# Kernel tuning notes

Measured on AMD Instinct MI355X. Metric: run time of the kernel, lower is better.

The kernel has to match this reference:

```python
import jax, jax.numpy as jnp
import numpy as np

N_NODES = 10000
N_EDGES = 160000
IN_DIM = 512
HID = 128
HEADS = 8
EMB = 256
NEG_SLOPE = 0.2  # PyG GATConv default


def setup_inputs() -> dict:
    key = jax.random.key(0)
    ks = jax.random.split(key, 12)
    x = jax.random.normal(ks[0], (N_NODES, IN_DIM), dtype=jnp.float32)
    edge_index = jax.random.randint(ks[1], (2, N_EDGES), 0, N_NODES, dtype=jnp.int64)
    s1 = 1.0 / np.sqrt(IN_DIM)
    s2 = 1.0 / np.sqrt(HEADS * HID)
    W1 = jax.random.normal(ks[2], (IN_DIM, HEADS * HID), dtype=jnp.float32) * s1
    a_src1 = jax.random.normal(ks[3], (HEADS, HID), dtype=jnp.float32) * s2
    a_dst1 = jax.random.normal(ks[4], (HEADS, HID), dtype=jnp.float32) * s2
    b1 = jnp.zeros((HEADS * HID,), dtype=jnp.float32)
    W2 = jax.random.normal(ks[5], (HEADS * HID, EMB), dtype=jnp.float32) * s2
    a_src2 = jax.random.normal(ks[6], (1, EMB), dtype=jnp.float32) * (1.0 / np.sqrt(EMB))
    a_dst2 = jax.random.normal(ks[7], (1, EMB), dtype=jnp.float32) * (1.0 / np.sqrt(EMB))
    b2 = jnp.zeros((EMB,), dtype=jnp.float32)
    return {"x": x, "edge_index": edge_index, "W1": W1, "a_src1": a_src1,
            "a_dst1": a_dst1, "b1": b1, "W2": W2, "a_src2": a_src2,
            "a_dst2": a_dst2, "b2": b2}


def gat_layer(h_in, src, dst, W, a_src, a_dst, b, concat, num_nodes):
    """PyG-style GATConv (eval mode, self-loops already in src/dst)."""
    H, C = a_src.shape
    h = (h_in @ W).reshape(num_nodes, H, C)            # [N, H, C]
    alpha_src = jnp.einsum('nhc,hc->nh', h, a_src)      # [N, H]
    alpha_dst = jnp.einsum('nhc,hc->nh', h, a_dst)      # [N, H]
    e = jax.nn.leaky_relu(alpha_src[src] + alpha_dst[dst], NEG_SLOPE)  # [E, H]
    # segment softmax over incoming edges of each destination node
    m = jax.ops.segment_max(e, dst, num_segments=num_nodes)            # [N, H]
    ex = jnp.exp(e - m[dst])
    denom = jax.ops.segment_sum(ex, dst, num_segments=num_nodes)       # [N, H]
    alpha = ex / denom[dst]                                            # [E, H]
    out = jax.ops.segment_sum(h[src] * alpha[:, :, None], dst,
                              num_segments=num_nodes)                  # [N, H, C]
    out = out.reshape(num_nodes, H * C) if concat else out.mean(axis=1)
    return out + b


def reference(x, edge_index, W1, a_src1, a_dst1, b1, W2, a_src2, a_dst2, b2):
    N = x.shape[0]
    loops = jnp.arange(N, dtype=edge_index.dtype)
    src = jnp.concatenate([edge_index[0], loops])
    dst = jnp.concatenate([edge_index[1], loops])
    h = gat_layer(x, src, dst, W1, a_src1, a_dst1, b1, concat=True, num_nodes=N)
    h = jax.nn.elu(h)  # dropout inactive in eval mode
    out = gat_layer(h, src, dst, W2, a_src2, a_dst2, b2, concat=False, num_nodes=N)
    return out
```

## Files before the change

kernel.cpp:

```cpp
#include <hip/hip_runtime.h>
#include <hip/hip_bf16.h>

typedef __attribute__((ext_vector_type(8))) short short8;
typedef __attribute__((ext_vector_type(4))) float floatx4;
typedef __attribute__((ext_vector_type(4))) unsigned short ushort4v;
typedef __attribute__((ext_vector_type(8))) unsigned short ushort8v;
typedef __attribute__((ext_vector_type(2))) unsigned int uint2v;
typedef __attribute__((ext_vector_type(4))) unsigned int uint4v;

#define NN 10000
#define E0 160000
#define ETOT (E0 + NN)
#define IN_DIM 512
#define HID1 1024
#define EMB 256
#define MPAD 10112
#define NX (NN * IN_DIM)
#define NW1 (IN_DIM * HID1)
#define NW2 (HID1 * EMB)
#define DETB 625

__device__ __forceinline__ float bf2f(unsigned short u) {
    unsigned v = ((unsigned)u) << 16;
    float f;
    __builtin_memcpy(&f, &v, 4);
    return f;
}
__device__ __forceinline__ float bflo(unsigned v) {
    unsigned x = v << 16;
    float f; __builtin_memcpy(&f, &x, 4);
    return f;
}
__device__ __forceinline__ float bfhi(unsigned v) {
    unsigned x = v & 0xffff0000u;
    float f; __builtin_memcpy(&f, &x, 4);
    return f;
}
__device__ __forceinline__ unsigned short f2bf(float f) {
    unsigned u;
    __builtin_memcpy(&u, &f, 4);
    unsigned lsb = (u >> 16) & 1;
    u += 0x7fff + lsb;
    return (unsigned short)(u >> 16);
}
__device__ __forceinline__ unsigned packbf(float lo, float hi) {
    return (unsigned)f2bf(lo) | ((unsigned)f2bf(hi) << 16);
}
__device__ __forceinline__ float loadf(const void* p, size_t i, int isf32) {
    if (isf32) return ((const float*)p)[i];
    return bf2f(((const unsigned short*)p)[i]);
}
__device__ __forceinline__ float lrelu(float e) { return e > 0.f ? e : 0.2f * e; }

__global__ void zero_kernel(int* p, int n) {
    int i = blockIdx.x * 256 + threadIdx.x;
    if (i < n) p[i] = 0;
}

__global__ __launch_bounds__(256) void probe_kernel(const int* ei32, const unsigned* xw,
                                                    int* eflag, int* isf32) {
    int t = threadIdx.x;
    if (blockIdx.x < DETB) {
        int i = blockIdx.x * 256 + t;
        int v = 0;
        int idx = 2 * i + 1;
        if (idx < 2 * E0) v = ei32[idx];
        unsigned long long any = __ballot(v != 0);
        if (any && (t & 63) == 0) atomicOr(eflag, 1);
    } else {
        __shared__ int cnt[256];
        int c = 0;
        #pragma unroll
        for (int j = 0; j < 16; ++j) {
            unsigned w = xw[t * 16 + j];
            int ex = (w >> 7) & 0xFF;
            if (ex >= 110 && ex <= 135) c++;
        }
        cnt[t] = c;
        __syncthreads();
        for (int off = 128; off > 0; off >>= 1) {
            if (t < off) cnt[t] += cnt[t + off];
            __syncthreads();
        }
        if (t == 0) *isf32 = (cnt[0] < 2048) ? 1 : 0;
    }
}

__device__ __forceinline__ int load_edge(const void* ei, long long idx, int m32) {
    if (m32) return ((const int*)ei)[idx];
    return (int)(((const long long*)ei)[idx]);
}

__global__ void count_kernel(const void* ei, const int* flag, int* counts) {
    int e = blockIdx.x * 256 + threadIdx.x;
    if (e < E0) {
        int m32 = (*flag != 0);
        int d = load_edge(ei, (long long)E0 + e, m32);
        if (d >= 0 && d < NN) atomicAdd(&counts[d], 1);
    }
}

__global__ __launch_bounds__(1024) void scan_kernel(const int* counts, int* offsets, int* cursor) {
    __shared__ int wsum[16];
    int t = threadIdx.x;
    int lane = t & 63, wv = t >> 6;
    int base = t * 10;
    int local[10];
    int s = 0;
    #pragma unroll
    for (int j = 0; j < 10; ++j) {
        int idx = base + j;
        int v = (idx < NN) ? (counts[idx] + 1) : 0;
        local[j] = v; s += v;
    }
    int v = s;
    #pragma unroll
    for (int d = 1; d < 64; d <<= 1) {
        int o = __shfl_up(v, d, 64);
        if (lane >= d) v += o;
    }
    if (lane == 63) wsum[wv] = v;
    __syncthreads();
    if (t < 16) {
        int w = wsum[t];
        #pragma unroll
        for (int d = 1; d < 16; d <<= 1) {
            int o = __shfl_up(w, d, 16);
            if (t >= d) w += o;
        }
        wsum[t] = w;
    }
    __syncthreads();
    int woff = (wv == 0) ? 0 : wsum[wv - 1];
    int run = woff + v - s;
    #pragma unroll
    for (int j = 0; j < 10; ++j) {
        int idx = base + j;
        if (idx < NN) { offsets[idx] = run; cursor[idx] = run; run += local[j]; }
    }
    if (t == 1023) offsets[NN] = wsum[15];
}

__global__ void scatter_kernel(const void* ei, const int* flag, int* cursor, int* csr_src) {
    int e = blockIdx.x * 256 + threadIdx.x;
    if (e >= ETOT) return;
    int m32 = (*flag != 0);
    int s, d;
    if (e < E0) { s = load_edge(ei, e, m32); d = load_edge(ei, (long long)E0 + e, m32); }
    else { s = d = e - E0; }
    if (s < 0) s = 0; if (s >= NN) s = NN - 1;
    if (d < 0) d = 0; if (d >= NN) d = NN - 1;
    int pos = atomicAdd(&cursor[d], 1);
    if (pos >= 0 && pos < ETOT) csr_src[pos] = s;
}

__global__ void convall_kernel(const void* x, const void* W1, const void* W2,
                               unsigned short* xb, unsigned short* W1t, unsigned short* W2t,
                               const int* isf32)
{
    int i = blockIdx.x * 256 + threadIdx.x;
    int f = *isf32;
    if (i < NX) { xb[i] = f2bf(loadf(x, i, f)); return; }
    i -= NX;
    if (i < NW1) {
        int r = i / HID1, c = i % HID1;
        W1t[(size_t)c * IN_DIM + r] = f2bf(loadf(W1, i, f));
        return;
    }
    i -= NW1;
    if (i < NW2) {
        int r = i / EMB, c = i % EMB;
        W2t[(size_t)c * HID1 + r] = f2bf(loadf(W2, i, f));
    }
}

template<bool OUTBF16>
__global__ __launch_bounds__(256) void gemm_tile(
    const unsigned short* __restrict__ A,
    const unsigned short* __restrict__ Bt,
    void* __restrict__ Cv,
    int N, int K)
{
    __shared__ unsigned short As[128 * 32];
    __shared__ unsigned short Bs[128 * 32];
    int t = threadIdx.x;
    int wave = t >> 6;
    int lane = t & 63;
    int quad = lane >> 4;
    int l16  = lane & 15;
    int mq = wave & 1, nq = wave >> 1;
    size_t mblk = (size_t)blockIdx.x * 128;
    size_t nblk = (size_t)blockIdx.y * 128;

    floatx4 acc[4][4];
    #pragma unroll
    for (int i = 0; i < 4; ++i)
        #pragma unroll
        for (int j = 0; j < 4; ++j)
            acc[i][j] = (floatx4){0.f, 0.f, 0.f, 0.f};

    const unsigned short* Abase = A + mblk * K;
    const unsigned short* Bbase = Bt + nblk * K;

    for (int kk = 0; kk < K; kk += 32) {
        __syncthreads();
        #pragma unroll
        for (int j = 0; j < 2; ++j) {
            int chunk = (wave << 7) + (j << 6) + lane;
            int r  = chunk >> 2;
            int cs = (chunk & 3) ^ (r & 3);
            const unsigned short* ga = Abase + (size_t)r * K + kk + cs * 8;
            const unsigned short* gb = Bbase + (size_t)r * K + kk + cs * 8;
            __builtin_amdgcn_global_load_lds(
                (const __attribute__((address_space(1))) void*)ga,
                (__attribute__((address_space(3))) void*)(As + (size_t)((wave << 7) + (j << 6)) * 8),
                16, 0, 0);
            __builtin_amdgcn_global_load_lds(
                (const __attribute__((address_space(1))) void*)gb,
                (__attribute__((address_space(3))) void*)(Bs + (size_t)((wave << 7) + (j << 6)) * 8),
                16, 0, 0);
        }
        __syncthreads();

        short8 af[4], bf[4];
        #pragma unroll
        for (int i = 0; i < 4; ++i) {
            int ar = mq * 64 + i * 16 + l16;
            int br = nq * 64 + i * 16 + l16;
            af[i] = *(const short8*)(const void*)(As + ar * 32 + (quad ^ (ar & 3)) * 8);
            bf[i] = *(const short8*)(const void*)(Bs + br * 32 + (quad ^ (br & 3)) * 8);
        }
        #pragma unroll
        for (int i = 0; i < 4; ++i)
            #pragma unroll
            for (int j = 0; j < 4; ++j)
                acc[i][j] = __builtin_amdgcn_mfma_f32_16x16x32_bf16(af[i], bf[j], acc[i][j], 0, 0, 0);
    }

    size_t crow0 = mblk + mq * 64 + quad * 4;
    size_t ccol0 = nblk + nq * 64 + l16;
    #pragma unroll
    for (int i = 0; i < 4; ++i) {
        #pragma unroll
        for (int r = 0; r < 4; ++r) {
            size_t row = crow0 + i * 16 + r;
            size_t b = row * N + ccol0;
            #pragma unroll
            for (int j = 0; j < 4; ++j) {
                if (OUTBF16) ((unsigned short*)Cv)[b + j * 16] = f2bf(acc[i][j][r]);
                else         ((float*)Cv)[b + j * 16] = acc[i][j][r];
            }
        }
    }
}

__global__ __launch_bounds__(256) void alpha1_kernel(
    const unsigned short* __restrict__ h1,
    const void* __restrict__ a_src, const void* __restrict__ a_dst,
    const int* __restrict__ isf32,
    float* __restrict__ as1, float* __restrict__ ad1)
{
    int n = blockIdx.x, t = threadIdx.x;
    int f = *isf32;
    ushort4v hv = *(const ushort4v*)(const void*)(h1 + (size_t)n * HID1 + t * 4);
    float ps = 0.f, pd = 0.f;
    #pragma unroll
    for (int i = 0; i < 4; ++i) {
        float h = bf2f(hv[i]);
        ps += h * loadf(a_src, t * 4 + i, f);
        pd += h * loadf(a_dst, t * 4 + i, f);
    }
    #pragma unroll
    for (int off = 1; off < 32; off <<= 1) {
        ps += __shfl_xor(ps, off, 64);
        pd += __shfl_xor(pd, off, 64);
    }
    if ((t & 31) == 0) {
        int h = t >> 5;
        as1[n * 8 + h] = ps;
        ad1[n * 8 + h] = pd;
    }
}

__global__ __launch_bounds__(256) void agg1_kernel(
    const unsigned short* __restrict__ h1, const int* __restrict__ offsets,
    const int* __restrict__ csr_src, const float* __restrict__ as1,
    const float* __restrict__ ad1, const void* __restrict__ b1,
    const int* __restrict__ isf32,
    unsigned short* __restrict__ hmid)
{
    int n = blockIdx.x, t = threadIdx.x;
    int f = *isf32;
    int beg = offsets[n], end = offsets[n + 1];
    if (beg < 0) beg = 0; if (end > ETOT) end = ETOT;
    int g = t >> 6;
    int u = t & 63;
    int c0 = u * 16;
    int hc = u >> 3;
    float ad = ad1[n * 8 + hc];
    const unsigned* rb = (const unsigned*)h1 + u * 8;

    float den = 0.f;
    float acc[16];
    #pragma unroll
    for (int j = 0; j < 16; ++j) acc[j] = 0.f;

    int i = beg + g;
    for (; i + 12 < end; i += 16) {
        int s0 = csr_src[i];      s0 &= 0x7fffffff; if (s0 >= NN) s0 = 0;
        int s1 = csr_src[i + 4];  s1 &= 0x7fffffff; if (s1 >= NN) s1 = 0;
        int s2 = csr_src[i + 8];  s2 &= 0x7fffffff; if (s2 >= NN) s2 = 0;
        int s3 = csr_src[i + 12]; s3 &= 0x7fffffff; if (s3 >= NN) s3 = 0;
        uint4v a0 = *(const uint4v*)(const void*)(rb + (size_t)s0 * 512);
        uint4v b0 = *(const uint4v*)(const void*)(rb + (size_t)s0 * 512 + 4);
        uint4v a1 = *(const uint4v*)(const void*)(rb + (size_t)s1 * 512);
        uint4v b1v = *(const uint4v*)(const void*)(rb + (size_t)s1 * 512 + 4);
        uint4v a2 = *(const uint4v*)(const void*)(rb + (size_t)s2 * 512);
        uint4v b2v = *(const uint4v*)(const void*)(rb + (size_t)s2 * 512 + 4);
        uint4v a3 = *(const uint4v*)(const void*)(rb + (size_t)s3 * 512);
        uint4v b3v = *(const uint4v*)(const void*)(rb + (size_t)s3 * 512 + 4);
        float w0 = __expf(lrelu(as1[s0 * 8 + hc] + ad));
        float w1 = __expf(lrelu(as1[s1 * 8 + hc] + ad));
        float w2 = __expf(lrelu(as1[s2 * 8 + hc] + ad));
        float w3 = __expf(lrelu(as1[s3 * 8 + hc] + ad));
        den += (w0 + w1) + (w2 + w3);
        #pragma unroll
        for (int q = 0; q < 4; ++q) {
            acc[2 * q]      += (bflo(a0[q]) * w0 + bflo(a1[q]) * w1) + (bflo(a2[q]) * w2 + bflo(a3[q]) * w3);
            acc[2 * q + 1]  += (bfhi(a0[q]) * w0 + bfhi(a1[q]) * w1) + (bfhi(a2[q]) * w2 + bfhi(a3[q]) * w3);
            acc[8 + 2 * q]  += (bflo(b0[q]) * w0 + bflo(b1v[q]) * w1) + (bflo(b2v[q]) * w2 + bflo(b3v[q]) * w3);
            acc[9 + 2 * q]  += (bfhi(b0[q]) * w0 + bfhi(b1v[q]) * w1) + (bfhi(b2v[q]) * w2 + bfhi(b3v[q]) * w3);
        }
    }
    for (; i + 4 < end; i += 8) {
        int s0 = csr_src[i];     s0 &= 0x7fffffff; if (s0 >= NN) s0 = 0;
        int s1 = csr_src[i + 4]; s1 &= 0x7fffffff; if (s1 >= NN) s1 = 0;
        uint4v a0 = *(const uint4v*)(const void*)(rb + (size_t)s0 * 512);
        uint4v b0 = *(const uint4v*)(const void*)(rb + (size_t)s0 * 512 + 4);
        uint4v a1 = *(const uint4v*)(const void*)(rb + (size_t)s1 * 512);
        uint4v b1v = *(const uint4v*)(const void*)(rb + (size_t)s1 * 512 + 4);
        float w0 = __expf(lrelu(as1[s0 * 8 + hc] + ad));
        float w1 = __expf(lrelu(as1[s1 * 8 + hc] + ad));
        den += w0 + w1;
        #pragma unroll
        for (int q = 0; q < 4; ++q) {
            acc[2 * q]      += bflo(a0[q]) * w0 + bflo(a1[q]) * w1;
            acc[2 * q + 1]  += bfhi(a0[q]) * w0 + bfhi(a1[q]) * w1;
            acc[8 + 2 * q]  += bflo(b0[q]) * w0 + bflo(b1v[q]) * w1;
            acc[9 + 2 * q]  += bfhi(b0[q]) * w0 + bfhi(b1v[q]) * w1;
        }
    }
    if (i < end) {
        int s0 = csr_src[i]; s0 &= 0x7fffffff; if (s0 >= NN) s0 = 0;
        uint4v a0 = *(const uint4v*)(const void*)(rb + (size_t)s0 * 512);
        uint4v b0 = *(const uint4v*)(const void*)(rb + (size_t)s0 * 512 + 4);
        float w0 = __expf(lrelu(as1[s0 * 8 + hc] + ad));
        den += w0;
        #pragma unroll
        for (int q = 0; q < 4; ++q) {
            acc[2 * q]      += bflo(a0[q]) * w0;
            acc[2 * q + 1]  += bfhi(a0[q]) * w0;
            acc[8 + 2 * q]  += bflo(b0[q]) * w0;
            acc[9 + 2 * q]  += bfhi(b0[q]) * w0;
        }
    }

    __shared__ float sh[3][64][17];
    if (g) {
        #pragma unroll
        for (int j = 0; j < 16; ++j) sh[g - 1][u][j] = acc[j];
        sh[g - 1][u][16] = den;
    }
    __syncthreads();
    if (g == 0) {
        den += sh[0][u][16] + sh[1][u][16] + sh[2][u][16];
        float rden = 1.0f / fmaxf(den, 1e-30f);
        uint4v oA, oB;
        #pragma unroll
        for (int q = 0; q < 4; ++q) {
            float v0 = (acc[2 * q]     + sh[0][u][2 * q]     + sh[1][u][2 * q]     + sh[2][u][2 * q])     * rden + loadf(b1, c0 + 2 * q, f);
            float v1 = (acc[2 * q + 1] + sh[0][u][2 * q + 1] + sh[1][u][2 * q + 1] + sh[2][u][2 * q + 1]) * rden + loadf(b1, c0 + 2 * q + 1, f);
            v0 = v0 > 0.f ? v0 : (__expf(v0) - 1.0f);
            v1 = v1 > 0.f ? v1 : (__expf(v1) - 1.0f);
            oA[q] = packbf(v0, v1);
            float u0 = (acc[8 + 2 * q] + sh[0][u][8 + 2 * q] + sh[1][u][8 + 2 * q] + sh[2][u][8 + 2 * q]) * rden + loadf(b1, c0 + 8 + 2 * q, f);
            float u1 = (acc[9 + 2 * q] + sh[0][u][9 + 2 * q] + sh[1][u][9 + 2 * q] + sh[2][u][9 + 2 * q]) * rden + loadf(b1, c0 + 9 + 2 * q, f);
            u0 = u0 > 0.f ? u0 : (__expf(u0) - 1.0f);
            u1 = u1 > 0.f ? u1 : (__expf(u1) - 1.0f);
            oB[q] = packbf(u0, u1);
        }
        unsigned* hw = (unsigned*)hmid;
        *(uint4v*)(void*)(hw + (size_t)n * 512 + u * 8)     = oA;
        *(uint4v*)(void*)(hw + (size_t)n * 512 + u * 8 + 4) = oB;
    }
}

__global__ __launch_bounds__(256) void alpha2_kernel(
    const unsigned short* __restrict__ h2,
    const void* __restrict__ a_src2, const void* __restrict__ a_dst2,
    const int* __restrict__ isf32,
    float* __restrict__ as2, float* __restrict__ ad2)
{
    int n = blockIdx.x, t = threadIdx.x;
    int f = *isf32;
    float v = bf2f(h2[(size_t)n * EMB + t]);
    float ps = v * loadf(a_src2, t, f);
    float pd = v * loadf(a_dst2, t, f);
    __shared__ float rs[256], rdm[256];
    rs[t] = ps; rdm[t] = pd;
    __syncthreads();
    for (int off = 128; off > 0; off >>= 1) {
        if (t < off) { rs[t] += rs[t + off]; rdm[t] += rdm[t + off]; }
        __syncthreads();
    }
    if (t == 0) { as2[n] = rs[0]; ad2[n] = rdm[0]; }
}

__global__ __launch_bounds__(256) void agg2_kernel(
    const unsigned short* __restrict__ h2, const int* __restrict__ offsets,
    const int* __restrict__ csr_src, const float* __restrict__ as2,
    const float* __restrict__ ad2, const void* __restrict__ b2,
    const int* __restrict__ isf32,
    float* __restrict__ out)
{
    int n = blockIdx.x, t = threadIdx.x;
    int f = *isf32;
    int beg = offsets[n], end = offsets[n + 1];
    if (beg < 0) beg = 0; if (end > ETOT) end = ETOT;
    int g = t >> 6;
    int u = t & 63;
    int c0 = u * 4;
    float adn = ad2[n];

    float den = 0.f;
    float acc[4];
    #pragma unroll
    for (int j = 0; j < 4; ++j) acc[j] = 0.f;

    int i = beg + g;
    for (; i + 12 < end; i += 16) {
        int s0 = csr_src[i];      s0 &= 0x7fffffff; if (s0 >= NN) s0 = 0;
        int s1 = csr_src[i + 4];  s1 &= 0x7fffffff; if (s1 >= NN) s1 = 0;
        int s2 = csr_src[i + 8];  s2 &= 0x7fffffff; if (s2 >= NN) s2 = 0;
        int s3 = csr_src[i + 12]; s3 &= 0x7fffffff; if (s3 >= NN) s3 = 0;
        ushort4v hv0 = *(const ushort4v*)(const void*)(h2 + (size_t)s0 * EMB + c0);
        ushort4v hv1 = *(const ushort4v*)(const void*)(h2 + (size_t)s1 * EMB + c0);
        ushort4v hv2 = *(const ushort4v*)(const void*)(h2 + (size_t)s2 * EMB + c0);
        ushort4v hv3 = *(const ushort4v*)(const void*)(h2 + (size_t)s3 * EMB + c0);
        float e0 = as2[s0] + adn;
        float e1 = as2[s1] + adn;
        float e2 = as2[s2] + adn;
        float e3 = as2[s3] + adn;
        e0 = e0 > 0.f ? e0 : 0.2f * e0;
        e1 = e1 > 0.f ? e1 : 0.2f * e1;
        e2 = e2 > 0.f ? e2 : 0.2f * e2;
        e3 = e3 > 0.f ? e3 : 0.2f * e3;
        float w0 = __expf(e0), w1 = __expf(e1), w2 = __expf(e2), w3 = __expf(e3);
        den += (w0 + w1) + (w2 + w3);
        #pragma unroll
        for (int j = 0; j < 4; ++j)
            acc[j] += (bf2f(hv0[j]) * w0 + bf2f(hv1[j]) * w1)
                    + (bf2f(hv2[j]) * w2 + bf2f(hv3[j]) * w3);
    }
    for (; i + 4 < end; i += 8) {
        int s0 = csr_src[i];     s0 &= 0x7fffffff; if (s0 >= NN) s0 = 0;
        int s1 = csr_src[i + 4]; s1 &= 0x7fffffff; if (s1 >= NN) s1 = 0;
        ushort4v hv0 = *(const ushort4v*)(const void*)(h2 + (size_t)s0 * EMB + c0);
        ushort4v hv1 = *(const ushort4v*)(const void*)(h2 + (size_t)s1 * EMB + c0);
        float e0 = as2[s0] + adn;
        float e1 = as2[s1] + adn;
        e0 = e0 > 0.f ? e0 : 0.2f * e0;
        e1 = e1 > 0.f ? e1 : 0.2f * e1;
        float w0 = __expf(e0), w1 = __expf(e1);
        den += w0 + w1;
        #pragma unroll
        for (int j = 0; j < 4; ++j)
            acc[j] += bf2f(hv0[j]) * w0 + bf2f(hv1[j]) * w1;
    }
    if (i < end) {
        int s0 = csr_src[i]; s0 &= 0x7fffffff; if (s0 >= NN) s0 = 0;
        ushort4v hv0 = *(const ushort4v*)(const void*)(h2 + (size_t)s0 * EMB + c0);
        float e0 = as2[s0] + adn;
        e0 = e0 > 0.f ? e0 : 0.2f * e0;
        float w0 = __expf(e0);
        den += w0;
        #pragma unroll
        for (int j = 0; j < 4; ++j) acc[j] += bf2f(hv0[j]) * w0;
    }

    __shared__ float accsh[4][64][5];
    __shared__ float densh[4][64];
    #pragma unroll
    for (int j = 0; j < 4; ++j) accsh[g][u][j] = acc[j];
    densh[g][u] = den;
    __syncthreads();
    if (g == 0) {
        float dtot = densh[0][u] + densh[1][u] + densh[2][u] + densh[3][u];
        float rden = 1.0f / fmaxf(dtot, 1e-30f);
        floatx4 o;
        #pragma unroll
        for (int j = 0; j < 4; ++j) {
            float v = (accsh[0][u][j] + accsh[1][u][j] + accsh[2][u][j] + accsh[3][u][j]) * rden;
            o[j] = v + loadf(b2, c0 + j, f);
        }
        *(floatx4*)(void*)(out + (size_t)n * EMB + c0) = o;
    }
}

extern "C" void kernel_launch(void* const* d_in, const int* in_sizes, int n_in,
                              void* d_out, int out_size, void* d_ws, size_t ws_size,
                              hipStream_t stream)
{
    const void* x      = d_in[0];
    const void* edge   = d_in[1];
    const void* W1     = d_in[2];
    const void* a_src1 = d_in[3];
    const void* a_dst1 = d_in[4];
    const void* b1     = d_in[5];
    const void* W2     = d_in[6];
    const void* a_src2 = d_in[7];
    const void* a_dst2 = d_in[8];
    const void* b2     = d_in[9];
    float* out = (float*)d_out;

    char* ws = (char*)d_ws;
    size_t off = 0;
    auto alloc = [&](size_t bytes) -> void* {
        void* p = ws + off;
        off += (bytes + 255) & ~(size_t)255;
        return p;
    };
    int*            counts = (int*)alloc((NN + 2) * 4);
    int*            offs   = (int*)alloc((NN + 1) * 4);
    int*            cursor = (int*)alloc(NN * 4);
    int*            csr    = (int*)alloc((size_t)ETOT * 4);
    float*          as1    = (float*)alloc((size_t)NN * 8 * 4);
    float*          ad1    = (float*)alloc((size_t)NN * 8 * 4);
    float*          as2    = (float*)alloc((size_t)NN * 4);
    float*          ad2    = (float*)alloc((size_t)NN * 4);
    unsigned short* xb     = (unsigned short*)alloc((size_t)MPAD * IN_DIM * 2);
    unsigned short* W1t    = (unsigned short*)alloc((size_t)IN_DIM * HID1 * 2);
    unsigned short* W2t    = (unsigned short*)alloc((size_t)HID1 * EMB * 2);
    unsigned short* h1b    = (unsigned short*)alloc((size_t)MPAD * HID1 * 2);
    unsigned short* hmid   = (unsigned short*)alloc((size_t)MPAD * HID1 * 2);
    unsigned short* h2b    = (unsigned short*)alloc((size_t)MPAD * EMB * 2);
    int* eflag = counts + NN;
    int* isf32 = counts + NN + 1;

    zero_kernel<<<(NN + 2 + 255) / 256, 256, 0, stream>>>(counts, NN + 2);
    probe_kernel<<<DETB + 1, 256, 0, stream>>>((const int*)edge, (const unsigned*)x, eflag, isf32);

    count_kernel<<<(E0 + 255) / 256, 256, 0, stream>>>(edge, eflag, counts);
    scan_kernel<<<1, 1024, 0, stream>>>(counts, offs, cursor);
    scatter_kernel<<<(ETOT + 255) / 256, 256, 0, stream>>>(edge, eflag, cursor, csr);

    convall_kernel<<<(NX + NW1 + NW2 + 255) / 256, 256, 0, stream>>>(
        x, W1, W2, xb, W1t, W2t, isf32);

    dim3 g1(MPAD / 128, HID1 / 128);
    gemm_tile<true><<<g1, 256, 0, stream>>>(xb, W1t, h1b, HID1, IN_DIM);

    alpha1_kernel<<<NN, 256, 0, stream>>>(h1b, a_src1, a_dst1, isf32, as1, ad1);
    agg1_kernel<<<NN, 256, 0, stream>>>(h1b, offs, csr, as1, ad1, b1, isf32, hmid);

    dim3 g2(MPAD / 128, EMB / 128);
    gemm_tile<true><<<g2, 256, 0, stream>>>(hmid, W2t, h2b, EMB, HID1);

    alpha2_kernel<<<NN, 256, 0, stream>>>(h2b, a_src2, a_dst2, isf32, as2, ad2);
    agg2_kernel<<<NN, 256, 0, stream>>>(h2b, offs, csr, as2, ad2, b2, isf32, out);
}
```

Measured before the change: 301.4 us.

## Split GAT aggregation work per wavefront by node and head/chunk

Both aggregation kernels now give each wavefront one node and one feature slice (one head of 128 channels in layer 1, one 64-channel chunk in layer 2). Four 16-lane groups stride over the edges and are combined with cross-lane shuffles instead of shared memory and a block barrier. This drops the LDS reduction and __syncthreads, cuts per-thread accumulator registers, and raises the block count. In exchange, CSR indices and attention logits are re-read once per head or chunk, and per-edge row reads are narrower (16 B in layer 1, 8 B in layer 2).

Measured after the change: 303.9 us. About the same (+0.8%).

```diff
diff --git a/kernel.cpp b/kernel.cpp
--- a/kernel.cpp
+++ b/kernel.cpp
@@ -289,109 +289,93 @@
     const int* __restrict__ isf32,
     unsigned short* __restrict__ hmid)
 {
-    int n = blockIdx.x, t = threadIdx.x;
+    int head = blockIdx.x & 7;
+    int ng   = blockIdx.x >> 3;
+    int n    = ng * 4 + (threadIdx.x >> 6);
+    if (n >= NN) return;
+    int lane = threadIdx.x & 63;
+    int q    = lane >> 4;
+    int sl   = lane & 15;
     int f = *isf32;
     int beg = offsets[n], end = offsets[n + 1];
     if (beg < 0) beg = 0; if (end > ETOT) end = ETOT;
-    int g = t >> 6;
-    int u = t & 63;
-    int c0 = u * 16;
-    int hc = u >> 3;
-    float ad = ad1[n * 8 + hc];
-    const unsigned* rb = (const unsigned*)h1 + u * 8;
+    float ad = ad1[n * 8 + head];
+    const unsigned* rb = (const unsigned*)h1 + head * 64 + sl * 4;
+    const float* asb = as1 + head;
 
     float den = 0.f;
-    float acc[16];
-    #pragma unroll
-    for (int j = 0; j < 16; ++j) acc[j] = 0.f;
-
-    int i = beg + g;
+    float acc[8];
+    #pragma unroll
+    for (int j = 0; j < 8; ++j) acc[j] = 0.f;
+
+    int i = beg + q;
     for (; i + 12 < end; i += 16) {
         int s0 = csr_src[i];      s0 &= 0x7fffffff; if (s0 >= NN) s0 = 0;
         int s1 = csr_src[i + 4];  s1 &= 0x7fffffff; if (s1 >= NN) s1 = 0;
         int s2 = csr_src[i + 8];  s2 &= 0x7fffffff; if (s2 >= NN) s2 = 0;
         int s3 = csr_src[i + 12]; s3 &= 0x7fffffff; if (s3 >= NN) s3 = 0;
-        uint4v a0 = *(const uint4v*)(const void*)(rb + (size_t)s0 * 512);
-        uint4v b0 = *(const uint4v*)(const void*)(rb + (size_t)s0 * 512 + 4);
-        uint4v a1 = *(const uint4v*)(const void*)(rb + (size_t)s1 * 512);
-        uint4v b1v = *(const uint4v*)(const void*)(rb + (size_t)s1 * 512 + 4);
-        uint4v a2 = *(const uint4v*)(const void*)(rb + (size_t)s2 * 512);
-        uint4v b2v = *(const uint4v*)(const void*)(rb + (size_t)s2 * 512 + 4);
-        uint4v a3 = *(const uint4v*)(const void*)(rb + (size_t)s3 * 512);
-        uint4v b3v = *(const uint4v*)(const void*)(rb + (size_t)s3 * 512 + 4);
-        float w0 = __expf(lrelu(as1[s0 * 8 + hc] + ad));
-        float w1 = __expf(lrelu(as1[s1 * 8 + hc] + ad));
-        float w2 = __expf(lrelu(as1[s2 * 8 + hc] + ad));
-        float w3 = __expf(lrelu(as1[s3 * 8 + hc] + ad));
+        uint4v v0 = *(const uint4v*)(const void*)(rb + (size_t)s0 * 512);
+        uint4v v1 = *(const uint4v*)(const void*)(rb + (size_t)s1 * 512);
+        uint4v v2 = *(const uint4v*)(const void*)(rb + (size_t)s2 * 512);
+        uint4v v3 = *(const uint4v*)(const void*)(rb + (size_t)s3 * 512);
+        float w0 = __expf(lrelu(asb[s0 * 8] + ad));
+        float w1 = __expf(lrelu(asb[s1 * 8] + ad));
+        float w2 = __expf(lrelu(asb[s2 * 8] + ad));
+        float w3 = __expf(lrelu(asb[s3 * 8] + ad));
         den += (w0 + w1) + (w2 + w3);
         #pragma unroll
-        for (int q = 0; q < 4; ++q) {
-            acc[2 * q]      += (bflo(a0[q]) * w0 + bflo(a1[q]) * w1) + (bflo(a2[q]) * w2 + bflo(a3[q]) * w3);
-            acc[2 * q + 1]  += (bfhi(a0[q]) * w0 + bfhi(a1[q]) * w1) + (bfhi(a2[q]) * w2 + bfhi(a3[q]) * w3);
-            acc[8 + 2 * q]  += (bflo(b0[q]) * w0 + bflo(b1v[q]) * w1) + (bflo(b2v[q]) * w2 + bflo(b3v[q]) * w3);
-            acc[9 + 2 * q]  += (bfhi(b0[q]) * w0 + bfhi(b1v[q]) * w1) + (bfhi(b2v[q]) * w2 + bfhi(b3v[q]) * w3);
+        for (int k = 0; k < 4; ++k) {
+            acc[2 * k]     += (bflo(v0[k]) * w0 + bflo(v1[k]) * w1) + (bflo(v2[k]) * w2 + bflo(v3[k]) * w3);
+            acc[2 * k + 1] += (bfhi(v0[k]) * w0 + bfhi(v1[k]) * w1) + (bfhi(v2[k]) * w2 + bfhi(v3[k]) * w3);
         }
     }
     for (; i + 4 < end; i += 8) {
         int s0 = csr_src[i];     s0 &= 0x7fffffff; if (s0 >= NN) s0 = 0;
         int s1 = csr_src[i + 4]; s1 &= 0x7fffffff; if (s1 >= NN) s1 = 0;
-        uint4v a0 = *(const uint4v*)(const void*)(rb + (size_t)s0 * 512);
-        uint4v b0 = *(const uint4v*)(const void*)(rb + (size_t)s0 * 512 + 4);
-        uint4v a1 = *(const uint4v*)(const void*)(rb + (size_t)s1 * 512);
-        uint4v b1v = *(const uint4v*)(const void*)(rb + (size_t)s1 * 512 + 4);
-        float w0 = __expf(lrelu(as1[s0 * 8 + hc] + ad));
-        float w1 = __expf(lrelu(as1[s1 * 8 + hc] + ad));
+        uint4v v0 = *(const uint4v*)(const void*)(rb + (size_t)s0 * 512);
+        uint4v v1 = *(const uint4v*)(const void*)(rb + (size_t)s1 * 512);
+        float w0 = __expf(lrelu(asb[s0 * 8] + ad));
+        float w1 = __expf(lrelu(asb[s1 * 8] + ad));
         den += w0 + w1;
         #pragma unroll
-        for (int q = 0; q < 4; ++q) {
-            acc[2 * q]      += bflo(a0[q]) * w0 + bflo(a1[q]) * w1;
-            acc[2 * q + 1]  += bfhi(a0[q]) * w0 + bfhi(a1[q]) * w1;
-            acc[8 + 2 * q]  += bflo(b0[q]) * w0 + bflo(b1v[q]) * w1;
-            acc[9 + 2 * q]  += bfhi(b0[q]) * w0 + bfhi(b1v[q]) * w1;
+        for (int k = 0; k < 4; ++k) {
+            acc[2 * k]     += bflo(v0[k]) * w0 + bflo(v1[k]) * w1;
+            acc[2 * k + 1] += bfhi(v0[k]) * w0 + bfhi(v1[k]) * w1;
         }
     }
     if (i < end) {
         int s0 = csr_src[i]; s0 &= 0x7fffffff; if (s0 >= NN) s0 = 0;
-        uint4v a0 = *(const uint4v*)(const void*)(rb + (size_t)s0 * 512);
-        uint4v b0 = *(const uint4v*)(const void*)(rb + (size_t)s0 * 512 + 4);
-        float w0 = __expf(lrelu(as1[s0 * 8 + hc] + ad));
+        uint4v v0 = *(const uint4v*)(const void*)(rb + (size_t)s0 * 512);
+        float w0 = __expf(lrelu(asb[s0 * 8] + ad));
         den += w0;
         #pragma unroll
-        for (int q = 0; q < 4; ++q) {
-            acc[2 * q]      += bflo(a0[q]) * w0;
-            acc[2 * q + 1]  += bfhi(a0[q]) * w0;
-            acc[8 + 2 * q]  += bflo(b0[q]) * w0;
-            acc[9 + 2 * q]  += bfhi(b0[q]) * w0;
-        }
-    }
-
-    __shared__ float sh[3][64][17];
-    if (g) {
-        #pragma unroll
-        for (int j = 0; j < 16; ++j) sh[g - 1][u][j] = acc[j];
-        sh[g - 1][u][16] = den;
-    }
-    __syncthreads();
-    if (g == 0) {
-        den += sh[0][u][16] + sh[1][u][16] + sh[2][u][16];
+        for (int k = 0; k < 4; ++k) {
+            acc[2 * k]     += bflo(v0[k]) * w0;
+            acc[2 * k + 1] += bfhi(v0[k]) * w0;
+        }
+    }
+
+    #pragma unroll
+    for (int j = 0; j < 8; ++j) {
+        acc[j] += __shfl_xor(acc[j], 16, 64);
+        acc[j] += __shfl_xor(acc[j], 32, 64);
+    }
+    den += __shfl_xor(den, 16, 64);
+    den += __shfl_xor(den, 32, 64);
+
+    if (q == 0) {
         float rden = 1.0f / fmaxf(den, 1e-30f);
-        uint4v oA, oB;
-        #pragma unroll
-        for (int q = 0; q < 4; ++q) {
-            float v0 = (acc[2 * q]     + sh[0][u][2 * q]     + sh[1][u][2 * q]     + sh[2][u][2 * q])     * rden + loadf(b1, c0 + 2 * q, f);
-            float v1 = (acc[2 * q + 1] + sh[0][u][2 * q + 1] + sh[1][u][2 * q + 1] + sh[2][u][2 * q + 1]) * rden + loadf(b1, c0 + 2 * q + 1, f);
+        int c0 = head * 128 + sl * 8;
+        uint4v o;
+        #pragma unroll
+        for (int k = 0; k < 4; ++k) {
+            float v0 = acc[2 * k]     * rden + loadf(b1, c0 + 2 * k, f);
+            float v1 = acc[2 * k + 1] * rden + loadf(b1, c0 + 2 * k + 1, f);
             v0 = v0 > 0.f ? v0 : (__expf(v0) - 1.0f);
             v1 = v1 > 0.f ? v1 : (__expf(v1) - 1.0f);
-            oA[q] = packbf(v0, v1);
-            float u0 = (acc[8 + 2 * q] + sh[0][u][8 + 2 * q] + sh[1][u][8 + 2 * q] + sh[2][u][8 + 2 * q]) * rden + loadf(b1, c0 + 8 + 2 * q, f);
-            float u1 = (acc[9 + 2 * q] + sh[0][u][9 + 2 * q] + sh[1][u][9 + 2 * q] + sh[2][u][9 + 2 * q]) * rden + loadf(b1, c0 + 9 + 2 * q, f);
-            u0 = u0 > 0.f ? u0 : (__expf(u0) - 1.0f);
-            u1 = u1 > 0.f ? u1 : (__expf(u1) - 1.0f);
-            oB[q] = packbf(u0, u1);
-        }
-        unsigned* hw = (unsigned*)hmid;
-        *(uint4v*)(void*)(hw + (size_t)n * 512 + u * 8)     = oA;
-        *(uint4v*)(void*)(hw + (size_t)n * 512 + u * 8 + 4) = oB;
+            o[k] = packbf(v0, v1);
+        }
+        *(uint4v*)(void*)((unsigned*)hmid + (size_t)n * 512 + head * 64 + sl * 4) = o;
     }
 }
 
@@ -423,86 +407,83 @@
     const int* __restrict__ isf32,
     float* __restrict__ out)
 {
-    int n = blockIdx.x, t = threadIdx.x;
+    int chunk = blockIdx.x & 3;
+    int ng    = blockIdx.x >> 2;
+    int n     = ng * 4 + (threadIdx.x >> 6);
+    if (n >= NN) return;
+    int lane = threadIdx.x & 63;
+    int q    = lane >> 4;
+    int sl   = lane & 15;
     int f = *isf32;
     int beg = offsets[n], end = offsets[n + 1];
     if (beg < 0) beg = 0; if (end > ETOT) end = ETOT;
-    int g = t >> 6;
-    int u = t & 63;
-    int c0 = u * 4;
     float adn = ad2[n];
+    const unsigned* rb = (const unsigned*)h2 + chunk * 32 + sl * 2;
 
     float den = 0.f;
     float acc[4];
     #pragma unroll
     for (int j = 0; j < 4; ++j) acc[j] = 0.f;
 
-    int i = beg + g;
+    int i = beg + q;
     for (; i + 12 < end; i += 16) {
         int s0 = csr_src[i];      s0 &= 0x7fffffff; if (s0 >= NN) s0 = 0;
         int s1 = csr_src[i + 4];  s1 &= 0x7fffffff; if (s1 >= NN) s1 = 0;
         int s2 = csr_src[i + 8];  s2 &= 0x7fffffff; if (s2 >= NN) s2 = 0;
         int s3 = csr_src[i + 12]; s3 &= 0x7fffffff; if (s3 >= NN) s3 = 0;
-        ushort4v hv0 = *(const ushort4v*)(const void*)(h2 + (size_t)s0 * EMB + c0);
-        ushort4v hv1 = *(const ushort4v*)(const void*)(h2 + (size_t)s1 * EMB + c0);
-        ushort4v hv2 = *(const ushort4v*)(const void*)(h2 + (size_t)s2 * EMB + c0);
-        ushort4v hv3 = *(const ushort4v*)(const void*)(h2 + (size_t)s3 * EMB + c0);
-        float e0 = as2[s0] + adn;
-        float e1 = as2[s1] + adn;
-        float e2 = as2[s2] + adn;
-        float e3 = as2[s3] + adn;
-        e0 = e0 > 0.f ? e0 : 0.2f * e0;
-        e1 = e1 > 0.f ? e1 : 0.2f * e1;
-        e2 = e2 > 0.f ? e2 : 0.2f * e2;
-        e3 = e3 > 0.f ? e3 : 0.2f * e3;
-        float w0 = __expf(e0), w1 = __expf(e1), w2 = __expf(e2), w3 = __expf(e3);
+        uint2v v0 = *(const uint2v*)(const void*)(rb + (size_t)s0 * 128);
+        uint2v v1 = *(const uint2v*)(const void*)(rb + (size_t)s1 * 128);
+        uint2v v2 = *(const uint2v*)(const void*)(rb + (size_t)s2 * 128);
+        uint2v v3 = *(const uint2v*)(const void*)(rb + (size_t)s3 * 128);
+        float w0 = __expf(lrelu(as2[s0] + adn));
+        float w1 = __expf(lrelu(as2[s1] + adn));
+        float w2 = __expf(lrelu(as2[s2] + adn));
+        float w3 = __expf(lrelu(as2[s3] + adn));
         den += (w0 + w1) + (w2 + w3);
-        #pragma unroll
-        for (int j = 0; j < 4; ++j)
-            acc[j] += (bf2f(hv0[j]) * w0 + bf2f(hv1[j]) * w1)
-                    + (bf2f(hv2[j]) * w2 + bf2f(hv3[j]) * w3);
+        acc[0] += (bflo(v0[0]) * w0 + bflo(v1[0]) * w1) + (bflo(v2[0]) * w2 + bflo(v3[0]) * w3);
+        acc[1] += (bfhi(v0[0]) * w0 + bfhi(v1[0]) * w1) + (bfhi(v2[0]) * w2 + bfhi(v3[0]) * w3);
+        acc[2] += (bflo(v0[1]) * w0 + bflo(v1[1]) * w1) + (bflo(v2[1]) * w2 + bflo(v3[1]) * w3);
+        acc[3] += (bfhi(v0[1]) * w0 + bfhi(v1[1]) * w1) + (bfhi(v2[1]) * w2 + bfhi(v3[1]) * w3);
     }
     for (; i + 4 < end; i += 8) {
         int s0 = csr_src[i];     s0 &= 0x7fffffff; if (s0 >= NN) s0 = 0;
         int s1 = csr_src[i + 4]; s1 &= 0x7fffffff; if (s1 >= NN) s1 = 0;
-        ushort4v hv0 = *(const ushort4v*)(const void*)(h2 + (size_t)s0 * EMB + c0);
-        ushort4v hv1 = *(const ushort4v*)(const void*)(h2 + (size_t)s1 * EMB + c0);
-        float e0 = as2[s0] + adn;
-        float e1 = as2[s1] + adn;
-        e0 = e0 > 0.f ? e0 : 0.2f * e0;
-        e1 = e1 > 0.f ? e1 : 0.2f * e1;
-        float w0 = __expf(e0), w1 = __expf(e1);
+        uint2v v0 = *(const uint2v*)(const void*)(rb + (size_t)s0 * 128);
+        uint2v v1 = *(const uint2v*)(const void*)(rb + (size_t)s1 * 128);
+        float w0 = __expf(lrelu(as2[s0] + adn));
+        float w1 = __expf(lrelu(as2[s1] + adn));
         den += w0 + w1;
-        #pragma unroll
-        for (int j = 0; j < 4; ++j)
-            acc[j] += bf2f(hv0[j]) * w0 + bf2f(hv1[j]) * w1;
+        acc[0] += bflo(v0[0]) * w0 + bflo(v1[0]) * w1;
+        acc[1] += bfhi(v0[0]) * w0 + bfhi(v1[0]) * w1;
+        acc[2] += bflo(v0[1]) * w0 + bflo(v1[1]) * w1;
+        acc[3] += bfhi(v0[1]) * w0 + bfhi(v1[1]) * w1;
     }
     if (i < end) {
         int s0 = csr_src[i]; s0 &= 0x7fffffff; if (s0 >= NN) s0 = 0;
-        ushort4v hv0 = *(const ushort4v*)(const void*)(h2 + (size_t)s0 * EMB + c0);
-        float e0 = as2[s0] + adn;
-        e0 = e0 > 0.f ? e0 : 0.2f * e0;
-        float w0 = __expf(e0);
+        uint2v v0 = *(const uint2v*)(const void*)(rb + (size_t)s0 * 128);
+        float w0 = __expf(lrelu(as2[s0] + adn));
         den += w0;
-        #pragma unroll
-        for (int j = 0; j < 4; ++j) acc[j] += bf2f(hv0[j]) * w0;
-    }
-
-    __shared__ float accsh[4][64][5];
-    __shared__ float densh[4][64];
-    #pragma unroll
-    for (int j = 0; j < 4; ++j) accsh[g][u][j] = acc[j];
-    densh[g][u] = den;
-    __syncthreads();
-    if (g == 0) {
-        float dtot = densh[0][u] + densh[1][u] + densh[2][u] + densh[3][u];
-        float rden = 1.0f / fmaxf(dtot, 1e-30f);
+        acc[0] += bflo(v0[0]) * w0;
+        acc[1] += bfhi(v0[0]) * w0;
+        acc[2] += bflo(v0[1]) * w0;
+        acc[3] += bfhi(v0[1]) * w0;
+    }
+
+    #pragma unroll
+    for (int j = 0; j < 4; ++j) {
+        acc[j] += __shfl_xor(acc[j], 16, 64);
+        acc[j] += __shfl_xor(acc[j], 32, 64);
+    }
+    den += __shfl_xor(den, 16, 64);
+    den += __shfl_xor(den, 32, 64);
+
+    if (q == 0) {
+        float rden = 1.0f / fmaxf(den, 1e-30f);
+        int c0 = chunk * 64 + sl * 4;
         floatx4 o;
         #pragma unroll
-        for (int j = 0; j < 4; ++j) {
-            float v = (accsh[0][u][j] + accsh[1][u][j] + accsh[2][u][j] + accsh[3][u][j]) * rden;
-            o[j] = v + loadf(b2, c0 + j, f);
-        }
+        for (int j = 0; j < 4; ++j)
+            o[j] = acc[j] * rden + loadf(b2, c0 + j, f);
         *(floatx4*)(void*)(out + (size_t)n * EMB + c0) = o;
     }
 }
@@ -561,11 +542,11 @@
     gemm_tile<true><<<g1, 256, 0, stream>>>(xb, W1t, h1b, HID1, IN_DIM);
 
     alpha1_kernel<<<NN, 256, 0, stream>>>(h1b, a_src1, a_dst1, isf32, as1, ad1);
-    agg1_kernel<<<NN, 256, 0, stream>>>(h1b, offs, csr, as1, ad1, b1, isf32, hmid);
+    agg1_kernel<<<(NN / 4) * 8, 256, 0, stream>>>(h1b, offs, csr, as1, ad1, b1, isf32, hmid);
 
     dim3 g2(MPAD / 128, EMB / 128);
     gemm_tile<true><<<g2, 256, 0, stream>>>(hmid, W2t, h2b, EMB, HID1);
 
     alpha2_kernel<<<NN, 256, 0, stream>>>(h2b, a_src2, a_dst2, isf32, as2, ad2);
-    agg2_kernel<<<NN, 256, 0, stream>>>(h2b, offs, csr, as2, ad2, b2, isf32, out);
-}
+    agg2_kernel<<<(NN / 4) * 4, 256, 0, stream>>>(h2b, offs, csr, as2, ad2, b2, isf32, out);
+}
```
